# Kernel tuning notes

Hardware: AMD Instinct MI355X
Metric: run time of the kernel (lower is better)

Reference implementation:

```python
import jax, jax.numpy as jnp
import numpy as np

SIM_LEN = 16   # simulation_length T
N_CORES = 4    # chain of cores; ChipLatency == pipeline depth == N_CORES


def setup_inputs() -> dict:
    key = jax.random.key(0)
    kx, kw, kb = jax.random.split(key, 3)
    B, N, C = 64, 2048, N_CORES
    x = jax.random.uniform(kx, (B, N), dtype=jnp.float32)          # analog input in [0,1)
    weights = jax.random.normal(kw, (C, N, N), dtype=jnp.float32) / np.float32(np.sqrt(N))
    biases = jax.random.normal(kb, (C, N), dtype=jnp.float32) * 0.01
    thresholds = jnp.ones((C,), dtype=jnp.float32)
    return {"x": x, "weights": weights, "biases": biases, "thresholds": thresholds}


def _uniform_spikes(x, n_spk, cycle, T):
    # faithful translation of to_uniform_spikes(tensor, cycle)
    mask = (n_spk != 0) & (n_spk != T) & (cycle < T)
    n_safe = jnp.maximum(n_spk, 1.0)
    spacing = T / n_safe
    res = mask & (jnp.floor(cycle / spacing) < n_safe) & (jnp.floor(jnp.mod(cycle, spacing)) == 0)
    res = res.astype(x.dtype)
    res = jnp.where(n_spk == T, jnp.ones_like(res), res)
    # zeros_in is fed for cycles >= T
    return jnp.where(cycle < T, res, jnp.zeros_like(res))


def reference(x, weights, biases, thresholds):
    T = SIM_LEN
    C, N, _ = weights.shape
    B = x.shape[0]
    cycles = C + T                      # latency + simulation_length
    n_spk = jnp.round(x * T)            # spike counts per neuron for Uniform coding
    thr = thresholds[:, None, None]     # [C,1,1]

    def step(carry, cycle):
        memb, buffers, counts = carry   # memb/buffers: [C,B,N], counts: [B,N]
        in_spikes = _uniform_spikes(x, n_spk, cycle, T)            # [B,N]
        # gather phase: core 0 reads input spike train, core k reads core k-1's
        # previous-cycle spike buffer (axon source spans)
        signals = jnp.concatenate([in_spikes[None], buffers[:-1]], axis=0)  # [C,B,N]
        # integrate: memb += signals @ core_params (+ hardware bias)
        memb = memb + jnp.einsum('cba,can->cbn', signals, weights) + biases[:, None, :]
        # fire: thresholding_mode '<' -> spike where threshold < memb; soft reset
        spikes = (thr < memb).astype(x.dtype)
        memb = memb - spikes * thr
        # scatter phase: spikes become next-cycle buffers; output spans read last core
        counts = counts + spikes[-1]
        return (memb, spikes, counts), None

    init = (jnp.zeros((C, B, N), x.dtype),
            jnp.zeros((C, B, N), x.dtype),
            jnp.zeros((B, N), x.dtype))
    (_, _, counts), _ = jax.lax.scan(step, init, jnp.arange(cycles))
    return counts / T                   # rate-coded output
```

## Files before the change

### kernel.cpp

```cpp
#include <hip/hip_runtime.h>
#include <cstdint>
#include <cstddef>


#define N_DIM 2048
#define B_DIM 64
#define C_DIM 4
#define T_SIM 16
#define CYCLES 20
#define M_ROWS (CYCLES * B_DIM)

using i32x4 = __attribute__((ext_vector_type(4))) int;
using u32x4 = __attribute__((ext_vector_type(4))) uint32_t;

static constexpr size_t WQ_CORE    = (size_t)128 * 32 * 4 * 1024;
static constexpr size_t SIG_OFF    = (size_t)C_DIM * WQ_CORE;
static constexpr size_t AMAT_BYTES = (size_t)M_ROWS * N_DIM;

__device__ __forceinline__ size_t apk_off(int m, int k) {
    return ((size_t)((m >> 4) * 32 + (k >> 6)) << 10)
         + (size_t)((((k >> 4) & 3) << 8) + ((m & 15) << 4) + (k & 15));
}

__device__ __forceinline__ void pack_unit(const float* __restrict__ wc,
                                          signed char* __restrict__ wqc,
                                          int unit, int l) {
    int ct = unit & 127;
    int ks = unit >> 7;
    int n     = ct * 16 + (l & 15);
    int abase = ks * 64 + ((l >> 4) << 4);
    size_t blk_base = (((size_t)ct * 32 + ks) * 4) * 1024 + (size_t)l * 16;

    u32x4 d0, d1, d2, d3;
    for (int j4 = 0; j4 < 4; ++j4) {
        uint32_t w0 = 0, w1 = 0, w2 = 0, w3 = 0;
        for (int i = 0; i < 4; ++i) {
            int a = abase + j4 * 4 + i;
            float wv = wc[(size_t)a * N_DIM + n];
            long long vi = llrintf(wv * 8589934592.0f);
            int v  = (int)vi;
            int b0 = (int)(signed char)(v & 255); v = (v - b0) >> 8;
            int b1 = (int)(signed char)(v & 255); v = (v - b1) >> 8;
            int b2 = (int)(signed char)(v & 255); v = (v - b2) >> 8;
            int b3 = v;
            w0 |= (uint32_t)(uint8_t)b0 << (8 * i);
            w1 |= (uint32_t)(uint8_t)b1 << (8 * i);
            w2 |= (uint32_t)(uint8_t)b2 << (8 * i);
            w3 |= (uint32_t)(uint8_t)b3 << (8 * i);
        }
        d0[j4] = w0; d1[j4] = w1; d2[j4] = w2; d3[j4] = w3;
    }
    *(u32x4*)(wqc + blk_base)        = d0;
    *(u32x4*)(wqc + blk_base + 1024) = d1;
    *(u32x4*)(wqc + blk_base + 2048) = d2;
    *(u32x4*)(wqc + blk_base + 3072) = d3;
}

__device__ __forceinline__ int in_spike(float xv, int cycle) {
    if (cycle >= T_SIM) return 0;
    float n_spk = rintf(xv * 16.0f);
    if (n_spk == 16.0f) return 1;
    if (n_spk == 0.0f)  return 0;
    float spacing = 16.0f / n_spk;
    float cf = (float)cycle;
    float q = floorf(cf / spacing);
    float r = fmodf(cf, spacing);
    return (q < n_spk && floorf(r) == 0.0f) ? 1 : 0;
}

__device__ __forceinline__ void gen_unit(const float* __restrict__ x,
                                         signed char* __restrict__ a0, int gid) {
    int e   = gid << 2;
    int row = e >> 11;
    int b = row / 20, t = row - b * 20;
    int n0 = e & 2047;
    const float4 xv = *(const float4*)(x + (size_t)b * N_DIM + n0);
    uint32_t s = (uint32_t)in_spike(xv.x, t)
               | ((uint32_t)in_spike(xv.y, t) << 8)
               | ((uint32_t)in_spike(xv.z, t) << 16)
               | ((uint32_t)in_spike(xv.w, t) << 24);
    *(uint32_t*)(a0 + apk_off(row, n0)) = s;
}

__global__ __launch_bounds__(256) void prep0(const float* __restrict__ w,
                                             signed char* __restrict__ wq,
                                             const float* __restrict__ x,
                                             signed char* __restrict__ a0) {
    int wg = blockIdx.x, tid = threadIdx.x;
    if (wg < 1024) {
        pack_unit(w, wq, (wg << 2) | (tid >> 6), tid & 63);
    } else {
        gen_unit(x, a0, (wg - 1024) * 256 + tid);
    }
}

__global__ __launch_bounds__(256, 2) void gemm_core(
        signed char* __restrict__ wq, const signed char* __restrict__ apk,
        const float* __restrict__ wts, const float* __restrict__ biases,
        const float* __restrict__ thresholds,
        signed char* __restrict__ a_next, float* __restrict__ out, int c)
{
    __shared__ __align__(16) signed char smem[42240];
    const int wg  = blockIdx.x;
    const int tid = threadIdx.x;
    const int wv  = tid >> 6;
    const int l   = tid & 63;

    if (wg >= 512) {
        pack_unit(wts + (size_t)(c + 1) * N_DIM * N_DIM,
                  wq + (size_t)(c + 1) * WQ_CORE,
                  ((wg - 512) << 2) | wv, l);
        return;
    }

    const int e8 = wg >> 6;
    const int s  = wg & 63;

    const signed char* asrc  = apk + ((size_t)(e8 * 10) * 32) * 1024;
    const signed char* b0src = wq + ((size_t)(c * 128 + s * 2) * 32) * 4096;
    const signed char* b1src = wq + ((size_t)(c * 128 + s * 2 + 1) * 32) * 4096;

    auto STAGE = [&](int buf, int ks) {
        signed char* dst = smem + buf * 18432;
        if (wv < 2) {
#pragma unroll
            for (int r = 0; r < 5; ++r) {
                int blk = wv * 5 + r;
                __builtin_amdgcn_global_load_lds(
                    (const __attribute__((address_space(1))) uint32_t*)
                        (asrc + ((size_t)blk * 32 + ks) * 1024 + l * 16),
                    (__attribute__((address_space(3))) uint32_t*)(dst + blk * 1024),
                    16, 0, 0);
            }
        } else {
            const signed char* bs = (wv == 2) ? b0src : b1src;
#pragma unroll
            for (int p = 0; p < 4; ++p) {
                __builtin_amdgcn_global_load_lds(
                    (const __attribute__((address_space(1))) uint32_t*)
                        (bs + (size_t)ks * 4096 + p * 1024 + l * 16),
                    (__attribute__((address_space(3))) uint32_t*)
                        (dst + 10240 + (wv - 2) * 4096 + p * 1024),
                    16, 0, 0);
            }
        }
    };

    const int nc  = wv & 1;
    const int mtb = (wv >> 1) * 5;

    i32x4 acc[5][4];
#pragma unroll
    for (int j = 0; j < 5; ++j)
#pragma unroll
        for (int p = 0; p < 4; ++p) acc[j][p] = i32x4{0, 0, 0, 0};

    STAGE(0, 0);
    __syncthreads();
    int cur = 0;

    for (int ks = 0; ks < 32; ++ks) {
        if (ks < 31) STAGE(cur ^ 1, ks + 1);
        const signed char* lb = smem + cur * 18432 + (size_t)l * 16;
        i32x4 bf0 = *(const i32x4*)(lb + 10240 + nc * 4096);
        i32x4 bf1 = *(const i32x4*)(lb + 10240 + nc * 4096 + 1024);
        i32x4 bf2 = *(const i32x4*)(lb + 10240 + nc * 4096 + 2048);
        i32x4 bf3 = *(const i32x4*)(lb + 10240 + nc * 4096 + 3072);
        __builtin_amdgcn_s_setprio(1);
#pragma unroll
        for (int j = 0; j < 5; ++j) {
            i32x4 af = *(const i32x4*)(lb + (mtb + j) * 1024);
            acc[j][0] = __builtin_amdgcn_mfma_i32_16x16x64_i8(af, bf0, acc[j][0], 0, 0, 0);
            acc[j][1] = __builtin_amdgcn_mfma_i32_16x16x64_i8(af, bf1, acc[j][1], 0, 0, 0);
            acc[j][2] = __builtin_amdgcn_mfma_i32_16x16x64_i8(af, bf2, acc[j][2], 0, 0, 0);
            acc[j][3] = __builtin_amdgcn_mfma_i32_16x16x64_i8(af, bf3, acc[j][3], 0, 0, 0);
        }
        __builtin_amdgcn_s_setprio(0);
        __syncthreads();
        cur ^= 1;
    }

    double* scr = (double*)smem;
    const int nl = nc * 16 + (l & 15);
#pragma unroll
    for (int j = 0; j < 5; ++j) {
#pragma unroll
        for (int r = 0; r < 4; ++r) {
            int rl = (mtb + j) * 16 + ((l >> 4) << 2) + r;
            long long comb = ((long long)acc[j][3][r] << 24) + ((long long)acc[j][2][r] << 16)
                           + ((long long)acc[j][1][r] << 8)  +  (long long)acc[j][0][r];
            scr[rl * 33 + nl] = (double)comb * (1.0 / 8589934592.0);
        }
    }
    __syncthreads();

    const int b_loc = tid >> 5;
    const int n_loc = tid & 31;
    const int b = e8 * 8 + b_loc;
    const int n = (s << 5) + n_loc;
    const double bv = (double)biases[c * N_DIM + n];
    const double th = (double)thresholds[c];
    double m = 0.0;
    float cnt = 0.0f;
    if (c < 3) a_next[apk_off(b * 20, n)] = 0;
    for (int t = 0; t < CYCLES; ++t) {
        m = m + scr[(b_loc * 20 + t) * 33 + n_loc] + bv;
        bool sp = (th < m);
        if (sp) m -= th;
        if (c < 3) {
            if (t + 1 < CYCLES) a_next[apk_off(b * 20 + t + 1, n)] = sp ? 1 : 0;
        } else if (sp) {
            cnt += 1.0f;
        }
    }
    if (c == 3) out[(size_t)b * N_DIM + n] = cnt * 0.0625f;
}

extern "C" void kernel_launch(void* const* d_in, const int* in_sizes, int n_in,
                              void* d_out, int out_size, void* d_ws, size_t ws_size,
                              hipStream_t stream) {
    const float* x       = (const float*)d_in[0];
    const float* wts     = (const float*)d_in[1];
    const float* biases  = (const float*)d_in[2];
    const float* thr     = (const float*)d_in[3];
    float* out           = (float*)d_out;

    signed char* wq  = (signed char*)d_ws;
    signed char* sig = (signed char*)((char*)d_ws + SIG_OFF);

    prep0<<<dim3(3584), dim3(256), 0, stream>>>(wts, wq, x, sig);

    for (int c = 0; c < C_DIM; ++c) {
        const signed char* a_cur = sig + (size_t)c * AMAT_BYTES;
        signed char* a_nxt = (c < 3) ? (signed char*)(sig + (size_t)(c + 1) * AMAT_BYTES)
                                     : (signed char*)sig;
        int grid = (c < 3) ? 1536 : 512;
        gemm_core<<<dim3(grid), dim3(256), 0, stream>>>(wq, a_cur, wts, biases,
                                                        thr, a_nxt, out, c);
    }
}
```

Baseline: 104.2 us.

## Fuse core-0 weight quantization into the first GEMM's B-tile staging

Core 0's weights are no longer packed into the int8 workspace by a separate prep kernel. A dedicated gemm_core0 kernel reads fp32 weights directly, quantizes them into four int8 byte planes in registers, and writes them to shared memory while waves 0-1 stage the A tile. It is software-pipelined across two register buffers. This removes the prep pass and its write/read round trip, but the B-loading waves now do strided fp32 global loads and quantization math inside the main loop, which may stall the MFMA pipeline.

Result: slower. 130.6 us (+25.3%).

```diff
diff --git a/kernel.cpp b/kernel.cpp
--- a/kernel.cpp
+++ b/kernel.cpp
@@ -20,6 +20,15 @@
 __device__ __forceinline__ size_t apk_off(int m, int k) {
     return ((size_t)((m >> 4) * 32 + (k >> 6)) << 10)
          + (size_t)((((k >> 4) & 3) << 8) + ((m & 15) << 4) + (k & 15));
+}
+
+__device__ __forceinline__ void quant4(float wv, int& b0, int& b1, int& b2, int& b3) {
+    long long vi = llrintf(wv * 8589934592.0f);
+    int v  = (int)vi;
+    b0 = (int)(signed char)(v & 255); v = (v - b0) >> 8;
+    b1 = (int)(signed char)(v & 255); v = (v - b1) >> 8;
+    b2 = (int)(signed char)(v & 255); v = (v - b2) >> 8;
+    b3 = v;
 }
 
 __device__ __forceinline__ void pack_unit(const float* __restrict__ wc,
@@ -36,13 +45,8 @@
         uint32_t w0 = 0, w1 = 0, w2 = 0, w3 = 0;
         for (int i = 0; i < 4; ++i) {
             int a = abase + j4 * 4 + i;
-            float wv = wc[(size_t)a * N_DIM + n];
-            long long vi = llrintf(wv * 8589934592.0f);
-            int v  = (int)vi;
-            int b0 = (int)(signed char)(v & 255); v = (v - b0) >> 8;
-            int b1 = (int)(signed char)(v & 255); v = (v - b1) >> 8;
-            int b2 = (int)(signed char)(v & 255); v = (v - b2) >> 8;
-            int b3 = v;
+            int b0, b1, b2, b3;
+            quant4(wc[(size_t)a * N_DIM + n], b0, b1, b2, b3);
             w0 |= (uint32_t)(uint8_t)b0 << (8 * i);
             w1 |= (uint32_t)(uint8_t)b1 << (8 * i);
             w2 |= (uint32_t)(uint8_t)b2 << (8 * i);
@@ -68,8 +72,9 @@
     return (q < n_spk && floorf(r) == 0.0f) ? 1 : 0;
 }
 
-__device__ __forceinline__ void gen_unit(const float* __restrict__ x,
-                                         signed char* __restrict__ a0, int gid) {
+__global__ __launch_bounds__(256) void gen_in(const float* __restrict__ x,
+                                              signed char* __restrict__ a0) {
+    int gid = blockIdx.x * 256 + threadIdx.x;
     int e   = gid << 2;
     int row = e >> 11;
     int b = row / 20, t = row - b * 20;
@@ -82,104 +87,11 @@
     *(uint32_t*)(a0 + apk_off(row, n0)) = s;
 }
 
-__global__ __launch_bounds__(256) void prep0(const float* __restrict__ w,
-                                             signed char* __restrict__ wq,
-                                             const float* __restrict__ x,
-                                             signed char* __restrict__ a0) {
-    int wg = blockIdx.x, tid = threadIdx.x;
-    if (wg < 1024) {
-        pack_unit(w, wq, (wg << 2) | (tid >> 6), tid & 63);
-    } else {
-        gen_unit(x, a0, (wg - 1024) * 256 + tid);
-    }
-}
-
-__global__ __launch_bounds__(256, 2) void gemm_core(
-        signed char* __restrict__ wq, const signed char* __restrict__ apk,
-        const float* __restrict__ wts, const float* __restrict__ biases,
-        const float* __restrict__ thresholds,
-        signed char* __restrict__ a_next, float* __restrict__ out, int c)
+__device__ __forceinline__ void epilogue(
+        signed char* smem, i32x4 (*acc)[4], int tid, int l, int nc, int mtb,
+        int e8, int s, const float* biases, const float* thresholds,
+        signed char* a_next, float* out, int c)
 {
-    __shared__ __align__(16) signed char smem[42240];
-    const int wg  = blockIdx.x;
-    const int tid = threadIdx.x;
-    const int wv  = tid >> 6;
-    const int l   = tid & 63;
-
-    if (wg >= 512) {
-        pack_unit(wts + (size_t)(c + 1) * N_DIM * N_DIM,
-                  wq + (size_t)(c + 1) * WQ_CORE,
-                  ((wg - 512) << 2) | wv, l);
-        return;
-    }
-
-    const int e8 = wg >> 6;
-    const int s  = wg & 63;
-
-    const signed char* asrc  = apk + ((size_t)(e8 * 10) * 32) * 1024;
-    const signed char* b0src = wq + ((size_t)(c * 128 + s * 2) * 32) * 4096;
-    const signed char* b1src = wq + ((size_t)(c * 128 + s * 2 + 1) * 32) * 4096;
-
-    auto STAGE = [&](int buf, int ks) {
-        signed char* dst = smem + buf * 18432;
-        if (wv < 2) {
-#pragma unroll
-            for (int r = 0; r < 5; ++r) {
-                int blk = wv * 5 + r;
-                __builtin_amdgcn_global_load_lds(
-                    (const __attribute__((address_space(1))) uint32_t*)
-                        (asrc + ((size_t)blk * 32 + ks) * 1024 + l * 16),
-                    (__attribute__((address_space(3))) uint32_t*)(dst + blk * 1024),
-                    16, 0, 0);
-            }
-        } else {
-            const signed char* bs = (wv == 2) ? b0src : b1src;
-#pragma unroll
-            for (int p = 0; p < 4; ++p) {
-                __builtin_amdgcn_global_load_lds(
-                    (const __attribute__((address_space(1))) uint32_t*)
-                        (bs + (size_t)ks * 4096 + p * 1024 + l * 16),
-                    (__attribute__((address_space(3))) uint32_t*)
-                        (dst + 10240 + (wv - 2) * 4096 + p * 1024),
-                    16, 0, 0);
-            }
-        }
-    };
-
-    const int nc  = wv & 1;
-    const int mtb = (wv >> 1) * 5;
-
-    i32x4 acc[5][4];
-#pragma unroll
-    for (int j = 0; j < 5; ++j)
-#pragma unroll
-        for (int p = 0; p < 4; ++p) acc[j][p] = i32x4{0, 0, 0, 0};
-
-    STAGE(0, 0);
-    __syncthreads();
-    int cur = 0;
-
-    for (int ks = 0; ks < 32; ++ks) {
-        if (ks < 31) STAGE(cur ^ 1, ks + 1);
-        const signed char* lb = smem + cur * 18432 + (size_t)l * 16;
-        i32x4 bf0 = *(const i32x4*)(lb + 10240 + nc * 4096);
-        i32x4 bf1 = *(const i32x4*)(lb + 10240 + nc * 4096 + 1024);
-        i32x4 bf2 = *(const i32x4*)(lb + 10240 + nc * 4096 + 2048);
-        i32x4 bf3 = *(const i32x4*)(lb + 10240 + nc * 4096 + 3072);
-        __builtin_amdgcn_s_setprio(1);
-#pragma unroll
-        for (int j = 0; j < 5; ++j) {
-            i32x4 af = *(const i32x4*)(lb + (mtb + j) * 1024);
-            acc[j][0] = __builtin_amdgcn_mfma_i32_16x16x64_i8(af, bf0, acc[j][0], 0, 0, 0);
-            acc[j][1] = __builtin_amdgcn_mfma_i32_16x16x64_i8(af, bf1, acc[j][1], 0, 0, 0);
-            acc[j][2] = __builtin_amdgcn_mfma_i32_16x16x64_i8(af, bf2, acc[j][2], 0, 0, 0);
-            acc[j][3] = __builtin_amdgcn_mfma_i32_16x16x64_i8(af, bf3, acc[j][3], 0, 0, 0);
-        }
-        __builtin_amdgcn_s_setprio(0);
-        __syncthreads();
-        cur ^= 1;
-    }
-
     double* scr = (double*)smem;
     const int nl = nc * 16 + (l & 15);
 #pragma unroll
@@ -216,6 +128,235 @@
     if (c == 3) out[(size_t)b * N_DIM + n] = cnt * 0.0625f;
 }
 
+__global__ __launch_bounds__(256, 2) void gemm_core(
+        signed char* __restrict__ wq, const signed char* __restrict__ apk,
+        const float* __restrict__ wts, const float* __restrict__ biases,
+        const float* __restrict__ thresholds,
+        signed char* __restrict__ a_next, float* __restrict__ out, int c)
+{
+    __shared__ __align__(16) signed char smem[42240];
+    const int wg  = blockIdx.x;
+    const int tid = threadIdx.x;
+    const int wv  = tid >> 6;
+    const int l   = tid & 63;
+
+    if (wg >= 512) {
+        pack_unit(wts + (size_t)(c + 1) * N_DIM * N_DIM,
+                  wq + (size_t)(c + 1) * WQ_CORE,
+                  ((wg - 512) << 2) | wv, l);
+        return;
+    }
+
+    const int e8 = wg >> 6;
+    const int s  = wg & 63;
+
+    const signed char* asrc  = apk + ((size_t)(e8 * 10) * 32) * 1024;
+    const signed char* b0src = wq + ((size_t)(c * 128 + s * 2) * 32) * 4096;
+    const signed char* b1src = wq + ((size_t)(c * 128 + s * 2 + 1) * 32) * 4096;
+
+    auto STAGE = [&](int buf, int ks) {
+        signed char* dst = smem + buf * 18432;
+        if (wv < 2) {
+#pragma unroll
+            for (int r = 0; r < 5; ++r) {
+                int blk = wv * 5 + r;
+                __builtin_amdgcn_global_load_lds(
+                    (const __attribute__((address_space(1))) uint32_t*)
+                        (asrc + ((size_t)blk * 32 + ks) * 1024 + l * 16),
+                    (__attribute__((address_space(3))) uint32_t*)(dst + blk * 1024),
+                    16, 0, 0);
+            }
+        } else {
+            const signed char* bs = (wv == 2) ? b0src : b1src;
+#pragma unroll
+            for (int p = 0; p < 4; ++p) {
+                __builtin_amdgcn_global_load_lds(
+                    (const __attribute__((address_space(1))) uint32_t*)
+                        (bs + (size_t)ks * 4096 + p * 1024 + l * 16),
+                    (__attribute__((address_space(3))) uint32_t*)
+                        (dst + 10240 + (wv - 2) * 4096 + p * 1024),
+                    16, 0, 0);
+            }
+        }
+    };
+
+    const int nc  = wv & 1;
+    const int mtb = (wv >> 1) * 5;
+
+    i32x4 acc[5][4];
+#pragma unroll
+    for (int j = 0; j < 5; ++j)
+#pragma unroll
+        for (int p = 0; p < 4; ++p) acc[j][p] = i32x4{0, 0, 0, 0};
+
+    STAGE(0, 0);
+    __syncthreads();
+    int cur = 0;
+
+    for (int ks = 0; ks < 32; ++ks) {
+        if (ks < 31) STAGE(cur ^ 1, ks + 1);
+        const signed char* lb = smem + cur * 18432 + (size_t)l * 16;
+        i32x4 bf0 = *(const i32x4*)(lb + 10240 + nc * 4096);
+        i32x4 bf1 = *(const i32x4*)(lb + 10240 + nc * 4096 + 1024);
+        i32x4 bf2 = *(const i32x4*)(lb + 10240 + nc * 4096 + 2048);
+        i32x4 bf3 = *(const i32x4*)(lb + 10240 + nc * 4096 + 3072);
+        __builtin_amdgcn_s_setprio(1);
+#pragma unroll
+        for (int j = 0; j < 5; ++j) {
+            i32x4 af = *(const i32x4*)(lb + (mtb + j) * 1024);
+            acc[j][0] = __builtin_amdgcn_mfma_i32_16x16x64_i8(af, bf0, acc[j][0], 0, 0, 0);
+            acc[j][1] = __builtin_amdgcn_mfma_i32_16x16x64_i8(af, bf1, acc[j][1], 0, 0, 0);
+            acc[j][2] = __builtin_amdgcn_mfma_i32_16x16x64_i8(af, bf2, acc[j][2], 0, 0, 0);
+            acc[j][3] = __builtin_amdgcn_mfma_i32_16x16x64_i8(af, bf3, acc[j][3], 0, 0, 0);
+        }
+        __builtin_amdgcn_s_setprio(0);
+        __syncthreads();
+        cur ^= 1;
+    }
+
+    epilogue(smem, acc, tid, l, nc, mtb, e8, s, biases, thresholds, a_next, out, c);
+}
+
+__global__ __launch_bounds__(256, 2) void gemm_core0(
+        signed char* __restrict__ wq, const signed char* __restrict__ apk,
+        const float* __restrict__ wts, const float* __restrict__ biases,
+        const float* __restrict__ thresholds,
+        signed char* __restrict__ a_next, float* __restrict__ out)
+{
+    __shared__ __align__(16) signed char smem[42240];
+    const int wg  = blockIdx.x;
+    const int tid = threadIdx.x;
+    const int wv  = tid >> 6;
+    const int l   = tid & 63;
+
+    if (wg >= 512) {
+        pack_unit(wts + (size_t)1 * N_DIM * N_DIM,
+                  wq + (size_t)1 * WQ_CORE,
+                  ((wg - 512) << 2) | wv, l);
+        return;
+    }
+
+    const int e8 = wg >> 6;
+    const int s  = wg & 63;
+    const int nc  = wv & 1;
+    const int mtb = (wv >> 1) * 5;
+
+    const signed char* asrc = apk + ((size_t)(e8 * 10) * 32) * 1024;
+    const int s2 = s * 2 + (wv - 2);
+    const float* bsrc32 = wts + (size_t)(((l >> 4) << 4)) * N_DIM
+                        + (wv >= 2 ? (s2 * 16 + (l & 15)) : 0);
+
+    auto STAGE_A = [&](int buf, int ks) {
+        signed char* dst = smem + buf * 18432;
+#pragma unroll
+        for (int r = 0; r < 5; ++r) {
+            int blk = wv * 5 + r;
+            __builtin_amdgcn_global_load_lds(
+                (const __attribute__((address_space(1))) uint32_t*)
+                    (asrc + ((size_t)blk * 32 + ks) * 1024 + l * 16),
+                (__attribute__((address_space(3))) uint32_t*)(dst + blk * 1024),
+                16, 0, 0);
+        }
+    };
+    auto LOADF = [&](float* f, int ks) {
+        const float* p = bsrc32 + (size_t)ks * 64 * N_DIM;
+#pragma unroll
+        for (int j = 0; j < 16; ++j) f[j] = p[(size_t)j * N_DIM];
+    };
+    auto QSTORE = [&](int buf, const float* f) {
+        signed char* dst = smem + buf * 18432 + 10240 + (wv - 2) * 4096 + l * 16;
+        u32x4 q0{0,0,0,0}, q1{0,0,0,0}, q2{0,0,0,0}, q3{0,0,0,0};
+#pragma unroll
+        for (int j = 0; j < 16; ++j) {
+            int b0, b1, b2, b3;
+            quant4(f[j], b0, b1, b2, b3);
+            const int d = j >> 2, sh = 8 * (j & 3);
+            q0[d] |= (uint32_t)(uint8_t)b0 << sh;
+            q1[d] |= (uint32_t)(uint8_t)b1 << sh;
+            q2[d] |= (uint32_t)(uint8_t)b2 << sh;
+            q3[d] |= (uint32_t)(uint8_t)b3 << sh;
+        }
+        *(u32x4*)(dst)        = q0;
+        *(u32x4*)(dst + 1024) = q1;
+        *(u32x4*)(dst + 2048) = q2;
+        *(u32x4*)(dst + 3072) = q3;
+    };
+
+    i32x4 acc[5][4];
+#pragma unroll
+    for (int j = 0; j < 5; ++j)
+#pragma unroll
+        for (int p = 0; p < 4; ++p) acc[j][p] = i32x4{0, 0, 0, 0};
+
+    float fA[16], fB[16];
+    if (wv < 2) {
+        STAGE_A(0, 0);
+    } else {
+        LOADF(fA, 0);
+        QSTORE(0, fA);
+        LOADF(fA, 1);
+    }
+    __syncthreads();
+    int cur = 0;
+
+#pragma unroll 1
+    for (int k2 = 0; k2 < 16; ++k2) {
+        const int ks = k2 * 2;
+        if (wv < 2) {
+            STAGE_A(cur ^ 1, ks + 1);
+        } else {
+            QSTORE(cur ^ 1, fA);
+            LOADF(fB, ks + 2 < 32 ? ks + 2 : 31);
+        }
+        {
+            const signed char* lb = smem + cur * 18432 + (size_t)l * 16;
+            i32x4 bf0 = *(const i32x4*)(lb + 10240 + nc * 4096);
+            i32x4 bf1 = *(const i32x4*)(lb + 10240 + nc * 4096 + 1024);
+            i32x4 bf2 = *(const i32x4*)(lb + 10240 + nc * 4096 + 2048);
+            i32x4 bf3 = *(const i32x4*)(lb + 10240 + nc * 4096 + 3072);
+            __builtin_amdgcn_s_setprio(1);
+#pragma unroll
+            for (int j = 0; j < 5; ++j) {
+                i32x4 af = *(const i32x4*)(lb + (mtb + j) * 1024);
+                acc[j][0] = __builtin_amdgcn_mfma_i32_16x16x64_i8(af, bf0, acc[j][0], 0, 0, 0);
+                acc[j][1] = __builtin_amdgcn_mfma_i32_16x16x64_i8(af, bf1, acc[j][1], 0, 0, 0);
+                acc[j][2] = __builtin_amdgcn_mfma_i32_16x16x64_i8(af, bf2, acc[j][2], 0, 0, 0);
+                acc[j][3] = __builtin_amdgcn_mfma_i32_16x16x64_i8(af, bf3, acc[j][3], 0, 0, 0);
+            }
+            __builtin_amdgcn_s_setprio(0);
+        }
+        __syncthreads();
+        cur ^= 1;
+        if (wv < 2) {
+            if (ks + 2 < 32) STAGE_A(cur ^ 1, ks + 2);
+        } else if (ks + 2 < 32) {
+            QSTORE(cur ^ 1, fB);
+            LOADF(fA, ks + 3 < 32 ? ks + 3 : 31);
+        }
+        {
+            const signed char* lb = smem + cur * 18432 + (size_t)l * 16;
+            i32x4 bf0 = *(const i32x4*)(lb + 10240 + nc * 4096);
+            i32x4 bf1 = *(const i32x4*)(lb + 10240 + nc * 4096 + 1024);
+            i32x4 bf2 = *(const i32x4*)(lb + 10240 + nc * 4096 + 2048);
+            i32x4 bf3 = *(const i32x4*)(lb + 10240 + nc * 4096 + 3072);
+            __builtin_amdgcn_s_setprio(1);
+#pragma unroll
+            for (int j = 0; j < 5; ++j) {
+                i32x4 af = *(const i32x4*)(lb + (mtb + j) * 1024);
+                acc[j][0] = __builtin_amdgcn_mfma_i32_16x16x64_i8(af, bf0, acc[j][0], 0, 0, 0);
+                acc[j][1] = __builtin_amdgcn_mfma_i32_16x16x64_i8(af, bf1, acc[j][1], 0, 0, 0);
+                acc[j][2] = __builtin_amdgcn_mfma_i32_16x16x64_i8(af, bf2, acc[j][2], 0, 0, 0);
+                acc[j][3] = __builtin_amdgcn_mfma_i32_16x16x64_i8(af, bf3, acc[j][3], 0, 0, 0);
+            }
+            __builtin_amdgcn_s_setprio(0);
+        }
+        __syncthreads();
+        cur ^= 1;
+    }
+
+    epilogue(smem, acc, tid, l, nc, mtb, e8, s, biases, thresholds, a_next, out, 0);
+}
+
 extern "C" void kernel_launch(void* const* d_in, const int* in_sizes, int n_in,
                               void* d_out, int out_size, void* d_ws, size_t ws_size,
                               hipStream_t stream) {
@@ -228,9 +369,12 @@
     signed char* wq  = (signed char*)d_ws;
     signed char* sig = (signed char*)((char*)d_ws + SIG_OFF);
 
-    prep0<<<dim3(3584), dim3(256), 0, stream>>>(wts, wq, x, sig);
-
-    for (int c = 0; c < C_DIM; ++c) {
+    gen_in<<<dim3(2560), dim3(256), 0, stream>>>(x, sig);
+
+    gemm_core0<<<dim3(1536), dim3(256), 0, stream>>>(
+        wq, sig, wts, biases, thr, sig + AMAT_BYTES, out);
+
+    for (int c = 1; c < C_DIM; ++c) {
         const signed char* a_cur = sig + (size_t)c * AMAT_BYTES;
         signed char* a_nxt = (c < 3) ? (signed char*)(sig + (size_t)(c + 1) * AMAT_BYTES)
                                      : (signed char*)sig;
```
